# Performance work log

Measured on AMD Instinct MI355X. Metric: run time of the kernel, lower is better.

## Reference

```python
import jax, jax.numpy as jnp
import numpy as np

N = 50000
E = 800000
IN_FEATS = 256
NUM_HEADS = 4
OUT_FEATS = 64
NUM_ETYPES = 8
ALPHA = 100.0
NEG_SLOPE_ATTN = 0.2   # self.leaky_relu
NEG_SLOPE_EW = 0.01    # nn.LeakyReLU() default, applied to edge weights


def leaky_relu(x, slope):
    return jnp.where(x >= 0, x, slope * x)


def setup_inputs() -> dict:
    key = jax.random.key(0)
    ks = jax.random.split(key, 8)
    feat = jax.random.normal(ks[0], (N, IN_FEATS), dtype=jnp.float32)
    src = jax.random.randint(ks[1], (E,), 0, N, dtype=jnp.int32)
    dst = jax.random.randint(ks[2], (E,), 0, N, dtype=jnp.int32)
    # etypes are 1-indexed in the original code (edge_weight[edge_feats - 1])
    edge_feats = jax.random.randint(ks[3], (E,), 1, NUM_ETYPES + 1, dtype=jnp.int32)
    # parameters (xavier-normal-ish init for weights; edge_weight = 1/alpha)
    fc_w = jax.random.normal(ks[4], (NUM_HEADS * OUT_FEATS, IN_FEATS), dtype=jnp.float32) * 0.05
    attn_l = jax.random.normal(ks[5], (1, NUM_HEADS, OUT_FEATS), dtype=jnp.float32) * 0.1
    attn_r = jax.random.normal(ks[6], (1, NUM_HEADS, OUT_FEATS), dtype=jnp.float32) * 0.1
    edge_weight = jnp.full((NUM_ETYPES, NUM_HEADS), 1.0 / ALPHA, dtype=jnp.float32)
    return {"feat": feat, "src": src, "dst": dst, "edge_feats": edge_feats,
            "fc_w": fc_w, "attn_l": attn_l, "attn_r": attn_r, "edge_weight": edge_weight}


def reference(feat, src, dst, edge_feats, fc_w, attn_l, attn_r, edge_weight):
    # feat: [N, F_in] -> ft: [N, H, D]
    ft = (feat @ fc_w.T).reshape(-1, NUM_HEADS, OUT_FEATS)
    el = jnp.einsum('nhd,ohd->nh', ft, attn_l)  # [N, H]
    er = jnp.einsum('nhd,ohd->nh', ft, attn_r)  # [N, H]
    # edge-type weights (1-indexed), scaled & leaky-relu'd
    ew = leaky_relu(edge_weight * ALPHA, NEG_SLOPE_EW)  # [T, H]
    ee = ew[edge_feats - 1]                              # [E, H]
    # per-edge logits: u_add_v, times edge weight, leaky relu
    e = leaky_relu((el[src] + er[dst]) * ee, NEG_SLOPE_ATTN)  # [E, H]
    # edge softmax grouped by destination node
    emax = jax.ops.segment_max(e, dst, num_segments=N)        # [N, H]
    ex = jnp.exp(e - emax[dst])
    denom = jax.ops.segment_sum(ex, dst, num_segments=N)      # [N, H]
    a = ex / denom[dst]                                        # [E, H]
    # weighted scatter-sum: sum over edges of a * ft[src]
    msg = ft[src] * a[:, :, None]                              # [E, H, D]
    rst = jax.ops.segment_sum(msg, dst, num_segments=N)       # [N, H, D]
    return rst
```

## Files before the change

kernel.cpp:

```cpp
#include <hip/hip_runtime.h>
#include <hip/hip_bf16.h>


#define NF 256
#define HD 256
#define NH 4
#define PB 256

typedef __attribute__((ext_vector_type(8))) short short8;
typedef __attribute__((ext_vector_type(4))) float f32x4;

static __device__ __forceinline__ unsigned short f2bf(float f) {
  unsigned int u = __float_as_uint(f);
  u += 0x7FFFu + ((u >> 16) & 1u);
  return (unsigned short)(u >> 16);
}
static __device__ __forceinline__ float bf2f(unsigned short s) {
  return __uint_as_float(((unsigned int)s) << 16);
}
static __device__ __forceinline__ unsigned pkbf(float a, float b) {
  __hip_bfloat162 h = __float22bfloat162_rn(make_float2(a, b));
  return *(unsigned*)&h;
}
static __device__ __forceinline__ float wcalc(float sum, float ew) {
  float x = sum * ew;
  x = (x >= 0.f) ? x : 0.2f * x;
  return __expf(x);
}
static __device__ __forceinline__ short8 cvt8(float4 x, float4 y) {
  union { short8 s; uint4 u; } cv;
  cv.u = make_uint4(pkbf(x.x, x.y), pkbf(x.z, x.w),
                    pkbf(y.x, y.y), pkbf(y.z, y.w));
  return cv.s;
}

static __device__ __forceinline__ void gemm_tile_direct(
    const float* __restrict__ feat, const float* __restrict__ fc_w,
    const float* __restrict__ attn_l, const float* __restrict__ attn_r,
    unsigned short* __restrict__ ftb, float* __restrict__ el,
    float* __restrict__ er, int n, int row0, int tid) {
  int lane = tid & 63, w = tid >> 6;
  int rr = lane & 15, kq = lane >> 4;
  f32x4 acc[4][4];
#pragma unroll
  for (int i = 0; i < 4; ++i)
#pragma unroll
    for (int j = 0; j < 4; ++j) acc[i][j] = (f32x4){0.f, 0.f, 0.f, 0.f};

  const float* ap[4];
#pragma unroll
  for (int rt = 0; rt < 4; ++rt) {
    int arow = row0 + rt * 16 + rr; if (arow >= n) arow = n - 1;
    ap[rt] = feat + (size_t)arow * NF + kq * 8;
  }
  const float* bp[4];
#pragma unroll
  for (int ct = 0; ct < 4; ++ct) {
    int bcol = w * 64 + ct * 16 + rr;
    bp[ct] = fc_w + (size_t)bcol * NF + kq * 8;
  }

#pragma unroll 2
  for (int kc = 0; kc < 8; ++kc) {
    short8 afr[4], bfr[4];
#pragma unroll
    for (int rt = 0; rt < 4; ++rt) {
      float4 x = *(const float4*)(ap[rt] + kc * 32);
      float4 y = *(const float4*)(ap[rt] + kc * 32 + 4);
      afr[rt] = cvt8(x, y);
    }
#pragma unroll
    for (int ct = 0; ct < 4; ++ct) {
      float4 x = *(const float4*)(bp[ct] + kc * 32);
      float4 y = *(const float4*)(bp[ct] + kc * 32 + 4);
      bfr[ct] = cvt8(x, y);
    }
#pragma unroll
    for (int rt = 0; rt < 4; ++rt)
#pragma unroll
      for (int ct = 0; ct < 4; ++ct)
        acc[rt][ct] = __builtin_amdgcn_mfma_f32_16x16x32_bf16(
            afr[rt], bfr[ct], acc[rt][ct], 0, 0, 0);
  }

  int ln = lane & 15, lq = lane >> 4;
  float al4[4], ar4[4];
#pragma unroll
  for (int ct = 0; ct < 4; ++ct) {
    al4[ct] = attn_l[w * 64 + ct * 16 + ln];
    ar4[ct] = attn_r[w * 64 + ct * 16 + ln];
  }
#pragma unroll
  for (int rt = 0; rt < 4; ++rt) {
#pragma unroll
    for (int r = 0; r < 4; ++r) {
      float pl = 0.f, pr = 0.f;
#pragma unroll
      for (int ct = 0; ct < 4; ++ct) {
        float v = acc[rt][ct][r];
        pl += v * al4[ct]; pr += v * ar4[ct];
      }
#pragma unroll
      for (int off = 1; off <= 8; off <<= 1) {
        pl += __shfl_xor(pl, off);
        pr += __shfl_xor(pr, off);
      }
      int row = row0 + rt * 16 + lq * 4 + r;
      if (row < n) {
        if (ln == 0) { el[row * NH + w] = pl; er[row * NH + w] = pr; }
        unsigned short* fr = ftb + (size_t)row * HD + w * 64 + ln;
#pragma unroll
        for (int ct = 0; ct < 4; ++ct) fr[ct * 16] = f2bf(acc[rt][ct][r]);
      }
    }
  }
}

__global__ __launch_bounds__(256) void hist_gemm_k(
    const int* __restrict__ dst, int* __restrict__ ghist, int e, int epb, int hb,
    const float* __restrict__ feat, const float* __restrict__ fc_w,
    const float* __restrict__ attn_l, const float* __restrict__ attn_r,
    unsigned short* __restrict__ ftb, float* __restrict__ el,
    float* __restrict__ er, int n, int tile0) {
  int tid = threadIdx.x;
  if (blockIdx.x < hb) {
    __shared__ int bins[256];
    int blk = blockIdx.x;
    bins[tid] = 0;
    __syncthreads();
    int e0 = blk * epb, e1 = e0 + epb; if (e1 > e) e1 = e;
    for (int i = e0 + tid; i < e1; i += 256)
      atomicAdd(&bins[dst[i] >> 8], 1);
    __syncthreads();
    ghist[blk * 256 + tid] = bins[tid];
    return;
  }
  gemm_tile_direct(feat, fc_w, attn_l, attn_r, ftb, el, er, n,
                   (tile0 + (int)blockIdx.x - hb) * 64, tid);
}

__global__ __launch_bounds__(256) void scan_k(
    const int* __restrict__ ghist, int* __restrict__ lsg,
    int* __restrict__ bb, int nblk) {
  int tid = threadIdx.x;
  int run = 0;
  int i = 0;
  for (; i + 8 <= nblk; i += 8) {
    int v[8];
#pragma unroll
    for (int j = 0; j < 8; ++j) v[j] = ghist[(i + j) * 256 + tid];
#pragma unroll
    for (int j = 0; j < 8; ++j) { lsg[(i + j) * 256 + tid] = run; run += v[j]; }
  }
  for (; i < nblk; ++i) {
    int v = ghist[i * 256 + tid];
    lsg[i * 256 + tid] = run;
    run += v;
  }
  __shared__ int wt[4];
  int lane = tid & 63, wid = tid >> 6;
  int inc = run;
#pragma unroll
  for (int off = 1; off < 64; off <<= 1) {
    int t = __shfl_up(inc, off);
    if (lane >= off) inc += t;
  }
  if (lane == 63) wt[wid] = inc;
  __syncthreads();
  int base = 0;
  if (wid > 0) base += wt[0];
  if (wid > 1) base += wt[1];
  if (wid > 2) base += wt[2];
  bb[tid] = base + inc - run;
  if (tid == 255) bb[256] = base + inc;
}

__global__ __launch_bounds__(256) void scat_gemm_k(
    const int* __restrict__ src, const int* __restrict__ dst,
    const int* __restrict__ efeats, const int* __restrict__ lsg,
    const int* __restrict__ bb, int* __restrict__ mid, int e, int epb, int sb,
    const float* __restrict__ feat, const float* __restrict__ fc_w,
    const float* __restrict__ attn_l, const float* __restrict__ attn_r,
    unsigned short* __restrict__ ftb, float* __restrict__ el,
    float* __restrict__ er, int n, int tile0) {
  int tid = threadIdx.x;
  if (blockIdx.x < sb) {
    __shared__ int cur[256];
    int blk = blockIdx.x;
    cur[tid] = bb[tid] + lsg[blk * 256 + tid];
    __syncthreads();
    int e0 = blk * epb, e1 = e0 + epb; if (e1 > e) e1 = e;
    for (int i = e0 + tid; i < e1; i += 256) {
      int d = dst[i];
      int pos = atomicAdd(&cur[d >> 8], 1);
      mid[pos] = src[i] | ((efeats[i] - 1) << 17) | ((d & 255) << 20);
    }
    return;
  }
  gemm_tile_direct(feat, fc_w, attn_l, attn_r, ftb, el, er, n,
                   (tile0 + (int)blockIdx.x - sb) * 64, tid);
}

__global__ __launch_bounds__(256) void bucket_k(
    const int* __restrict__ mid, const int* __restrict__ bb,
    int* __restrict__ poffs, int* __restrict__ pk, int nN) {
  __shared__ int cnt[256];
  __shared__ int cur[256];
  int tid = threadIdx.x, b = blockIdx.x;
  int bb0 = bb[b];
  int bb1 = bb[b + 1];
  cnt[tid] = 0;
  __syncthreads();
  for (int i = bb0 + tid; i < bb1; i += 256)
    atomicAdd(&cnt[(mid[i] >> 20) & 255], 1);
  __syncthreads();
  if (tid < 64) {
    int carry = 0;
#pragma unroll
    for (int c = 0; c < 4; ++c) {
      int v = cnt[c * 64 + tid];
      int inc = v;
#pragma unroll
      for (int off = 1; off < 64; off <<= 1) {
        int t2 = __shfl_up(inc, off);
        if (tid >= off) inc += t2;
      }
      cur[c * 64 + tid] = inc - v + carry;
      carry += __shfl(inc, 63);
    }
  }
  __syncthreads();
  int node = b * 256 + tid;
  int g = bb0 + cur[tid];
  if (node <= nN) poffs[node] = g;
  cur[tid] = g;
  __syncthreads();
  for (int i = bb0 + tid; i < bb1; i += 256) {
    int v = mid[i];
    int pos = atomicAdd(&cur[(v >> 20) & 255], 1);
    pk[pos] = v & 0xFFFFF;
  }
}

__global__ __launch_bounds__(256) void agg3_k(
    const unsigned short* __restrict__ ftb, const int* __restrict__ pk,
    const float* __restrict__ el, const float* __restrict__ er,
    const float* __restrict__ ewt, const int* __restrict__ offs,
    float* __restrict__ out, int n) {
  __shared__ float ew_s[32];
  if (threadIdx.x < 32) {
    float v = ewt[threadIdx.x] * 100.0f;
    ew_s[threadIdx.x] = (v >= 0.f) ? v : 0.01f * v;
  }
  __syncthreads();
  int node = blockIdx.x * 4 + (threadIdx.x >> 6);
  int lane = threadIdx.x & 63;
  if (node >= n) return;
  int start = offs[node];
  int deg = offs[node + 1] - start;
  float o0 = 0.f, o1 = 0.f, o2 = 0.f, o3 = 0.f;
  if (deg > 0) {
    int hl = lane >> 4;
    float er_h = er[(size_t)node * NH + hl];
    const unsigned short* fb = ftb + (size_t)lane * 4;
    const float* elh = el + hl;
    const int* pg = pk + start;
    float ss = 0.f;
    int i = 0;
    for (; i + 8 <= deg; i += 8) {
      int4 pa = *(const int4*)(pg + i);
      int4 pb = *(const int4*)(pg + i + 4);
      int sA = pa.x & 0x1FFFF, tA = pa.x >> 17;
      int sB = pa.y & 0x1FFFF, tB = pa.y >> 17;
      int sC = pa.z & 0x1FFFF, tC = pa.z >> 17;
      int sD = pa.w & 0x1FFFF, tD = pa.w >> 17;
      int sE = pb.x & 0x1FFFF, tE = pb.x >> 17;
      int sF = pb.y & 0x1FFFF, tF = pb.y >> 17;
      int sG = pb.z & 0x1FFFF, tG = pb.z >> 17;
      int sH = pb.w & 0x1FFFF, tH = pb.w >> 17;
      float eA = elh[sA * NH], eB = elh[sB * NH], eC = elh[sC * NH], eD = elh[sD * NH];
      float eE = elh[sE * NH], eF = elh[sF * NH], eG = elh[sG * NH], eH = elh[sH * NH];
      ushort4 fA = *(const ushort4*)(fb + (size_t)sA * HD);
      ushort4 fB = *(const ushort4*)(fb + (size_t)sB * HD);
      ushort4 fC = *(const ushort4*)(fb + (size_t)sC * HD);
      ushort4 fD = *(const ushort4*)(fb + (size_t)sD * HD);
      ushort4 fE = *(const ushort4*)(fb + (size_t)sE * HD);
      ushort4 fF = *(const ushort4*)(fb + (size_t)sF * HD);
      ushort4 fG = *(const ushort4*)(fb + (size_t)sG * HD);
      ushort4 fH = *(const ushort4*)(fb + (size_t)sH * HD);
      float wA = wcalc(eA + er_h, ew_s[tA * NH + hl]);
      float wB = wcalc(eB + er_h, ew_s[tB * NH + hl]);
      float wC = wcalc(eC + er_h, ew_s[tC * NH + hl]);
      float wD = wcalc(eD + er_h, ew_s[tD * NH + hl]);
      float wE = wcalc(eE + er_h, ew_s[tE * NH + hl]);
      float wF = wcalc(eF + er_h, ew_s[tF * NH + hl]);
      float wG = wcalc(eG + er_h, ew_s[tG * NH + hl]);
      float wH = wcalc(eH + er_h, ew_s[tH * NH + hl]);
      ss += ((wA + wB) + (wC + wD)) + ((wE + wF) + (wG + wH));
      o0 = fmaf(wA, bf2f(fA.x), o0); o1 = fmaf(wA, bf2f(fA.y), o1);
      o2 = fmaf(wA, bf2f(fA.z), o2); o3 = fmaf(wA, bf2f(fA.w), o3);
      o0 = fmaf(wB, bf2f(fB.x), o0); o1 = fmaf(wB, bf2f(fB.y), o1);
      o2 = fmaf(wB, bf2f(fB.z), o2); o3 = fmaf(wB, bf2f(fB.w), o3);
      o0 = fmaf(wC, bf2f(fC.x), o0); o1 = fmaf(wC, bf2f(fC.y), o1);
      o2 = fmaf(wC, bf2f(fC.z), o2); o3 = fmaf(wC, bf2f(fC.w), o3);
      o0 = fmaf(wD, bf2f(fD.x), o0); o1 = fmaf(wD, bf2f(fD.y), o1);
      o2 = fmaf(wD, bf2f(fD.z), o2); o3 = fmaf(wD, bf2f(fD.w), o3);
      o0 = fmaf(wE, bf2f(fE.x), o0); o1 = fmaf(wE, bf2f(fE.y), o1);
      o2 = fmaf(wE, bf2f(fE.z), o2); o3 = fmaf(wE, bf2f(fE.w), o3);
      o0 = fmaf(wF, bf2f(fF.x), o0); o1 = fmaf(wF, bf2f(fF.y), o1);
      o2 = fmaf(wF, bf2f(fF.z), o2); o3 = fmaf(wF, bf2f(fF.w), o3);
      o0 = fmaf(wG, bf2f(fG.x), o0); o1 = fmaf(wG, bf2f(fG.y), o1);
      o2 = fmaf(wG, bf2f(fG.z), o2); o3 = fmaf(wG, bf2f(fG.w), o3);
      o0 = fmaf(wH, bf2f(fH.x), o0); o1 = fmaf(wH, bf2f(fH.y), o1);
      o2 = fmaf(wH, bf2f(fH.z), o2); o3 = fmaf(wH, bf2f(fH.w), o3);
    }
    for (; i < deg; ++i) {
      int pv = pg[i];
      int sA = pv & 0x1FFFF, tA = pv >> 17;
      float eA = elh[sA * NH];
      ushort4 fA = *(const ushort4*)(fb + (size_t)sA * HD);
      float wA = wcalc(eA + er_h, ew_s[tA * NH + hl]);
      ss += wA;
      o0 = fmaf(wA, bf2f(fA.x), o0); o1 = fmaf(wA, bf2f(fA.y), o1);
      o2 = fmaf(wA, bf2f(fA.z), o2); o3 = fmaf(wA, bf2f(fA.w), o3);
    }
    float rs = 1.0f / ss;
    o0 *= rs; o1 *= rs; o2 *= rs; o3 *= rs;
  }
  *(float4*)(out + (size_t)node * HD + lane * 4) = make_float4(o0, o1, o2, o3);
}

extern "C" void kernel_launch(void* const* d_in, const int* in_sizes, int n_in,
                              void* d_out, int out_size, void* d_ws, size_t ws_size,
                              hipStream_t stream) {
  const float* feat   = (const float*)d_in[0];
  const int*   src    = (const int*)d_in[1];
  const int*   dst    = (const int*)d_in[2];
  const int*   efeats = (const int*)d_in[3];
  const float* fc_w   = (const float*)d_in[4];
  const float* attn_l = (const float*)d_in[5];
  const float* attn_r = (const float*)d_in[6];
  const float* ewt    = (const float*)d_in[7];
  float* out = (float*)d_out;

  int N = in_sizes[0] / NF;
  int E = in_sizes[1];

  char* ws = (char*)d_ws;
  size_t off = 0;
  unsigned short* ftb = (unsigned short*)(ws + off); off += (size_t)N * HD * 2;
  float* el  = (float*)(ws + off);  off += (size_t)N * NH * 4;
  float* er  = (float*)(ws + off);  off += (size_t)N * NH * 4;
  int* poffs = (int*)(ws + off);    off += ((size_t)N + 16) * 4;
  int* ghist = (int*)(ws + off);    off += (size_t)PB * 256 * 4;
  int* lsg   = (int*)(ws + off);    off += (size_t)PB * 256 * 4;
  int* bb    = (int*)(ws + off);    off += 260 * 4;
  int* mid   = (int*)(ws + off);    off += (size_t)E * 4;
  int* pk    = (int*)(ws + off);    off += (size_t)E * 4;

  int gb = (N + 63) / 64;
  int g1 = gb / 2;
  int g2 = gb - g1;
  int epb = (E + PB - 1) / PB;
  int nbuck = (N + 255) >> 8;

  hist_gemm_k<<<PB + g1, 256, 0, stream>>>(dst, ghist, E, epb, PB,
                                           feat, fc_w, attn_l, attn_r,
                                           ftb, el, er, N, 0);
  scan_k<<<1, 256, 0, stream>>>(ghist, lsg, bb, PB);
  scat_gemm_k<<<PB + g2, 256, 0, stream>>>(src, dst, efeats, lsg, bb, mid,
                                           E, epb, PB,
                                           feat, fc_w, attn_l, attn_r,
                                           ftb, el, er, N, g1);
  bucket_k<<<nbuck, 256, 0, stream>>>(mid, bb, poffs, pk, N);
  agg3_k<<<(N + 3) / 4, 256, 0, stream>>>(ftb, pk, el, er, ewt, poffs, out, N);
}
```

Before: 283.9 us.

## Stage GEMM operands through LDS in MFMA fragment layout and rebalance tile split

The fused GEMM tile used to load and convert A and B fragments straight from global memory in every wave, so all four waves re-read the same feature rows. Now each block cooperatively converts a 64-row A chunk and the 256-column B chunk to bf16 once and stores them in LDS in MFMA fragment order, with barriers around each K step of 64. The split of GEMM tiles between the histogram and scatter kernels also moves from half to a fixed 430. This adds about 40KB of LDS per block, which may lower occupancy for the histogram/scatter blocks that share the kernel, and adds two barriers per K step.

After: 249.9 us. -12.0%, faster.

```diff
diff --git a/kernel.cpp b/kernel.cpp
--- a/kernel.cpp
+++ b/kernel.cpp
@@ -34,53 +34,69 @@
   return cv.s;
 }
 
-static __device__ __forceinline__ void gemm_tile_direct(
+static __device__ __forceinline__ void gemm_tile(
     const float* __restrict__ feat, const float* __restrict__ fc_w,
     const float* __restrict__ attn_l, const float* __restrict__ attn_r,
     unsigned short* __restrict__ ftb, float* __restrict__ el,
-    float* __restrict__ er, int n, int row0, int tid) {
+    float* __restrict__ er, int n, int row0, int tid,
+    short* aF, short* bF) {
   int lane = tid & 63, w = tid >> 6;
-  int rr = lane & 15, kq = lane >> 4;
+
   f32x4 acc[4][4];
 #pragma unroll
   for (int i = 0; i < 4; ++i)
 #pragma unroll
     for (int j = 0; j < 4; ++j) acc[i][j] = (f32x4){0.f, 0.f, 0.f, 0.f};
 
-  const float* ap[4];
-#pragma unroll
-  for (int rt = 0; rt < 4; ++rt) {
-    int arow = row0 + rt * 16 + rr; if (arow >= n) arow = n - 1;
-    ap[rt] = feat + (size_t)arow * NF + kq * 8;
-  }
-  const float* bp[4];
-#pragma unroll
-  for (int ct = 0; ct < 4; ++ct) {
-    int bcol = w * 64 + ct * 16 + rr;
-    bp[ct] = fc_w + (size_t)bcol * NF + kq * 8;
-  }
-
-#pragma unroll 2
-  for (int kc = 0; kc < 8; ++kc) {
-    short8 afr[4], bfr[4];
-#pragma unroll
-    for (int rt = 0; rt < 4; ++rt) {
-      float4 x = *(const float4*)(ap[rt] + kc * 32);
-      float4 y = *(const float4*)(ap[rt] + kc * 32 + 4);
-      afr[rt] = cvt8(x, y);
-    }
-#pragma unroll
-    for (int ct = 0; ct < 4; ++ct) {
-      float4 x = *(const float4*)(bp[ct] + kc * 32);
-      float4 y = *(const float4*)(bp[ct] + kc * 32 + 4);
-      bfr[ct] = cvt8(x, y);
-    }
-#pragma unroll
-    for (int rt = 0; rt < 4; ++rt)
+  int ar = tid >> 2, ak = (tid & 3) << 4;
+  int arow = row0 + ar; if (arow >= n) arow = n - 1;
+  const float* ap = feat + (size_t)arow * NF + ak;
+  int am = ar & 15, art = ar >> 4;
+  int s0 = ak >> 5, q0 = (ak >> 3) & 3;
+  int s1 = (ak + 8) >> 5, q1 = ((ak + 8) >> 3) & 3;
+  short* aw0 = &aF[(((art * 2 + s0) * 64) + q0 * 16 + am) * 8];
+  short* aw1 = &aF[(((art * 2 + s1) * 64) + q1 * 16 + am) * 8];
+
+  const float* bp = fc_w + (size_t)tid * NF;
+  int bn = tid & 15, bcg = tid >> 4;
+
+  for (int k0 = 0; k0 < NF; k0 += 64) {
+    float4 f0 = *(const float4*)(ap + k0);
+    float4 f1 = *(const float4*)(ap + k0 + 4);
+    float4 f2 = *(const float4*)(ap + k0 + 8);
+    float4 f3 = *(const float4*)(ap + k0 + 12);
+    uint4 oa = make_uint4(pkbf(f0.x, f0.y), pkbf(f0.z, f0.w),
+                          pkbf(f1.x, f1.y), pkbf(f1.z, f1.w));
+    uint4 ob = make_uint4(pkbf(f2.x, f2.y), pkbf(f2.z, f2.w),
+                          pkbf(f3.x, f3.y), pkbf(f3.z, f3.w));
+    *(uint4*)aw0 = oa;
+    *(uint4*)aw1 = ob;
+#pragma unroll
+    for (int o8 = 0; o8 < 8; ++o8) {
+      float4 bx = *(const float4*)(bp + k0 + o8 * 8);
+      float4 by = *(const float4*)(bp + k0 + o8 * 8 + 4);
+      short8 bv = cvt8(bx, by);
+      int bs = o8 >> 2, bq = o8 & 3;
+      *(short8*)&bF[(((bcg * 2 + bs) * 64) + bq * 16 + bn) * 8] = bv;
+    }
+    __syncthreads();
+#pragma unroll
+    for (int s = 0; s < 2; ++s) {
+      short8 af[4], bfr[4];
+#pragma unroll
+      for (int rt = 0; rt < 4; ++rt)
+        af[rt] = *(const short8*)&aF[(((rt * 2 + s) * 64) + lane) * 8];
 #pragma unroll
       for (int ct = 0; ct < 4; ++ct)
-        acc[rt][ct] = __builtin_amdgcn_mfma_f32_16x16x32_bf16(
-            afr[rt], bfr[ct], acc[rt][ct], 0, 0, 0);
+        bfr[ct] = *(const short8*)&bF[((((w * 4 + ct) * 2 + s) * 64) + lane) * 8];
+#pragma unroll
+      for (int rt = 0; rt < 4; ++rt)
+#pragma unroll
+        for (int ct = 0; ct < 4; ++ct)
+          acc[rt][ct] = __builtin_amdgcn_mfma_f32_16x16x32_bf16(
+              af[rt], bfr[ct], acc[rt][ct], 0, 0, 0);
+    }
+    __syncthreads();
   }
 
   int ln = lane & 15, lq = lane >> 4;
@@ -121,10 +137,12 @@
     const float* __restrict__ feat, const float* __restrict__ fc_w,
     const float* __restrict__ attn_l, const float* __restrict__ attn_r,
     unsigned short* __restrict__ ftb, float* __restrict__ el,
-    float* __restrict__ er, int n, int tile0) {
+    float* __restrict__ er, int n) {
+  __shared__ short aF[4 * 2 * 64 * 8];
+  __shared__ short bF[16 * 2 * 64 * 8];
   int tid = threadIdx.x;
   if (blockIdx.x < hb) {
-    __shared__ int bins[256];
+    int* bins = (int*)aF;
     int blk = blockIdx.x;
     bins[tid] = 0;
     __syncthreads();
@@ -135,8 +153,8 @@
     ghist[blk * 256 + tid] = bins[tid];
     return;
   }
-  gemm_tile_direct(feat, fc_w, attn_l, attn_r, ftb, el, er, n,
-                   (tile0 + (int)blockIdx.x - hb) * 64, tid);
+  gemm_tile(feat, fc_w, attn_l, attn_r, ftb, el, er, n,
+            ((int)blockIdx.x - hb) * 64, tid, aF, bF);
 }
 
 __global__ __launch_bounds__(256) void scan_k(
@@ -183,9 +201,11 @@
     const float* __restrict__ attn_l, const float* __restrict__ attn_r,
     unsigned short* __restrict__ ftb, float* __restrict__ el,
     float* __restrict__ er, int n, int tile0) {
+  __shared__ short aF[4 * 2 * 64 * 8];
+  __shared__ short bF[16 * 2 * 64 * 8];
   int tid = threadIdx.x;
   if (blockIdx.x < sb) {
-    __shared__ int cur[256];
+    int* cur = (int*)aF;
     int blk = blockIdx.x;
     cur[tid] = bb[tid] + lsg[blk * 256 + tid];
     __syncthreads();
@@ -197,8 +217,8 @@
     }
     return;
   }
-  gemm_tile_direct(feat, fc_w, attn_l, attn_r, ftb, el, er, n,
-                   (tile0 + (int)blockIdx.x - sb) * 64, tid);
+  gemm_tile(feat, fc_w, attn_l, attn_r, ftb, el, er, n,
+            (tile0 + (int)blockIdx.x - sb) * 64, tid, aF, bF);
 }
 
 __global__ __launch_bounds__(256) void bucket_k(
@@ -359,14 +379,14 @@
   int* pk    = (int*)(ws + off);    off += (size_t)E * 4;
 
   int gb = (N + 63) / 64;
-  int g1 = gb / 2;
+  int g1 = 430;
   int g2 = gb - g1;
   int epb = (E + PB - 1) / PB;
   int nbuck = (N + 255) >> 8;
 
   hist_gemm_k<<<PB + g1, 256, 0, stream>>>(dst, ghist, E, epb, PB,
                                            feat, fc_w, attn_l, attn_r,
-                                           ftb, el, er, N, 0);
+                                           ftb, el, er, N);
   scan_k<<<1, 256, 0, stream>>>(ghist, lsg, bb, PB);
   scat_gemm_k<<<PB + g2, 256, 0, stream>>>(src, dst, efeats, lsg, bb, mid,
                                            E, epb, PB,
```
